# Optimization experiments

Measured on AMD Instinct MI355X. Metric: run time of the kernel, lower is better.

## Reference

```python
import jax, jax.numpy as jnp
import numpy as np

EMBED_DIM = 768
NUM_HEADS = 12
DILATION_RATES = [1, 2, 4]
SEGMENT_LENGTHS = [2048, 4096, 8192]
LN_EPS = 1e-5
CAUSAL = False


def _dilated_attention(q, k, v, causal=False):
    # q, k, v: (b, N, h, d)
    b, N, h, d = q.shape
    g = len(DILATION_RATES)
    gs = h // g
    scale = 1.0 / jnp.sqrt(jnp.asarray(d, q.dtype))
    out = jnp.zeros_like(q)
    for i, (r, s) in enumerate(zip(DILATION_RATES, SEGMENT_LENGTHS)):
        n = N // s
        offset = i % r
        hmin, hmax = i * gs, (i + 1) * gs
        # strided gather: (b, n, s_eff, gs, d)
        qi = q.reshape(b, n, s, h, d)[:, :, offset::r, hmin:hmax, :]
        ki = k.reshape(b, n, s, h, d)[:, :, offset::r, hmin:hmax, :]
        vi = v.reshape(b, n, s, h, d)[:, :, offset::r, hmin:hmax, :]
        scores = jnp.einsum('bnqhd,bnkhd->bnhqk', qi, ki) * scale
        if causal:
            s_eff = qi.shape[2]
            mask = jnp.tril(jnp.ones((s_eff, s_eff), dtype=bool))
            scores = jnp.where(mask, scores, jnp.asarray(-jnp.inf, scores.dtype))
        p = jax.nn.softmax(scores, axis=-1)
        x = jnp.einsum('bnhqk,bnkhd->bnqhd', p, vi)
        # original normalization: divide by sum over (segment, position) dims
        x = x / x.sum(axis=(1, 2), keepdims=True)
        out = (out.reshape(b, n, s, h, d)
                  .at[:, :, offset::r, hmin:hmax, :].add(x)
                  .reshape(b, N, h, d))
    return out / g


def setup_inputs() -> dict:
    key = jax.random.key(0)
    ks = jax.random.split(key, 13)
    b, N, E = 2, 8192, EMBED_DIM
    sd = 1.0 / np.sqrt(E)
    return {
        'query': jax.random.normal(ks[0], (b, N, E), jnp.float32),
        'key': jax.random.normal(ks[1], (b, N, E), jnp.float32),
        'value': jax.random.normal(ks[2], (b, N, E), jnp.float32),
        'Wq': jax.random.normal(ks[3], (E, E), jnp.float32) * sd,
        'bq': jnp.zeros((E,), jnp.float32),
        'Wk': jax.random.normal(ks[4], (E, E), jnp.float32) * sd,
        'bk': jnp.zeros((E,), jnp.float32),
        'Wv': jax.random.normal(ks[5], (E, E), jnp.float32) * sd,
        'bv': jnp.zeros((E,), jnp.float32),
        'Wo': jax.random.normal(ks[6], (E, E), jnp.float32) * sd,
        'bo': jnp.zeros((E,), jnp.float32),
        'ln_w': jnp.ones((E,), jnp.float32),
        'ln_b': jnp.zeros((E,), jnp.float32),
    }


def reference(query, key, value, Wq, bq, Wk, bk, Wv, bv, Wo, bo, ln_w, ln_b):
    b, N, E = query.shape
    h = NUM_HEADS
    d = E // h
    q = (query @ Wq + bq).reshape(b, N, h, d)
    k = (key @ Wk + bk).reshape(b, N, h, d)
    v = (value @ Wv + bv).reshape(b, N, h, d)
    x = _dilated_attention(q, k, v, causal=CAUSAL).reshape(b, N, E)
    mu = x.mean(axis=-1, keepdims=True)
    var = x.var(axis=-1, keepdims=True)
    x = (x - mu) / jnp.sqrt(var + LN_EPS) * ln_w + ln_b
    return x @ Wo + bo
```

## Files before the change

### kernel.cpp

```cpp
#include <hip/hip_runtime.h>

typedef __attribute__((ext_vector_type(4))) float f32x4;
typedef __attribute__((ext_vector_type(4))) unsigned int u32x4;
typedef __attribute__((ext_vector_type(8))) _Float16 half8;
typedef __attribute__((ext_vector_type(2))) _Float16 half2v;

__device__ inline f32x4 mfma_fp16(half8 a, half8 b, f32x4 c) {
  return __builtin_amdgcn_mfma_f32_16x16x32_f16(a, b, c, 0, 0, 0);
}

__device__ inline int kva(int row, int colbyte) {
  return ((row * 128 + colbyte) ^ ((row & 7) << 4)) >> 1;
}

__device__ inline void gload16(const _Float16* g, _Float16* l) {
  __builtin_amdgcn_global_load_lds(
      (const __attribute__((address_space(1))) void*)g,
      (__attribute__((address_space(3))) void*)l, 16, 0, 0);
}

__global__ __launch_bounds__(256) void wsplit4_kernel(
    const float* __restrict__ Wq, const float* __restrict__ Wk,
    const float* __restrict__ Wv, const float* __restrict__ Wo,
    _Float16* __restrict__ Whi, _Float16* __restrict__ Wlo) {
  int w = blockIdx.y;
  const float* W = (w == 0) ? Wq : (w == 1) ? Wk : (w == 2) ? Wv : Wo;
  int i = blockIdx.x * 256 + threadIdx.x;
  int k = i / 768, n = i % 768;
  float v = W[i];
  _Float16 h = (_Float16)v;
  Whi[w * 589824 + n * 768 + k] = h;
  Wlo[w * 589824 + n * 768 + k] = (_Float16)(v - (float)h);
}

__device__ inline void asplit_body(const float* __restrict__ A,
                                   _Float16* __restrict__ Ahi,
                                   _Float16* __restrict__ Alo, int i) {
  f32x4 x0 = *(const f32x4*)(A + i);
  f32x4 x1 = *(const f32x4*)(A + i + 4);
  half8 vh, vl;
#pragma unroll
  for (int j = 0; j < 4; ++j) {
    _Float16 h0 = (_Float16)x0[j];
    vh[j] = h0; vl[j] = (_Float16)(x0[j] - (float)h0);
    _Float16 h1 = (_Float16)x1[j];
    vh[4 + j] = h1; vl[4 + j] = (_Float16)(x1[j] - (float)h1);
  }
  *(half8*)(Ahi + i) = vh;
  *(half8*)(Alo + i) = vl;
}

__global__ __launch_bounds__(256) void asplit_kernel(const float* __restrict__ A,
                                                     _Float16* __restrict__ Ahi,
                                                     _Float16* __restrict__ Alo) {
  asplit_body(A, Ahi, Alo, (blockIdx.x * 256 + threadIdx.x) * 8);
}

__global__ __launch_bounds__(256) void asplit3_kernel(
    const float* __restrict__ Aq, const float* __restrict__ Ak,
    const float* __restrict__ Av,
    _Float16* __restrict__ Aqh, _Float16* __restrict__ Aql,
    _Float16* __restrict__ Akh, _Float16* __restrict__ Akl,
    _Float16* __restrict__ Avh, _Float16* __restrict__ Avl) {
  int w = blockIdx.y;
  const float* A = (w == 0) ? Aq : (w == 1) ? Ak : Av;
  _Float16* H = (w == 0) ? Aqh : (w == 1) ? Akh : Avh;
  _Float16* L = (w == 0) ? Aql : (w == 1) ? Akl : Avl;
  asplit_body(A, H, L, (blockIdx.x * 256 + threadIdx.x) * 8);
}

__device__ inline int vt_base(int b, int h) {
  int base = b * 3670016;
  if (h < 4)      base += h * 524288;
  else if (h < 8) base += 2097152 + (h - 4) * 262144;
  else            base += 3145728 + (h - 8) * 131072;
  return base;
}

__device__ __forceinline__ void gemm3_core(
    const _Float16* __restrict__ Ahi, const _Float16* __restrict__ Alo,
    const _Float16* __restrict__ Bhi, const _Float16* __restrict__ Blo,
    const float* __restrict__ bias, _Float16* __restrict__ Chi,
    _Float16* __restrict__ Clo, int mode, int m0, int n0,
    _Float16* Ah, _Float16* Al, _Float16* Bh, _Float16* Bl) {
  int tid = threadIdx.x;
  int lane = tid & 63, wid = tid >> 6;
  int wm = wid >> 1, wn = wid & 1;
  int lg = lane >> 4, lc = lane & 15;

  f32x4 acc[2][4] = {};

  size_t sA[2], sB[2];
  int ldst[2];
#pragma unroll
  for (int c = 0; c < 2; ++c) {
    int idxv = c * 512 + tid;
    int m = idxv >> 3;
    int ke = ((idxv & 7) << 3) ^ ((m & 7) << 3);
    sA[c] = (size_t)(m0 + m) * 768 + ke;
    sB[c] = (size_t)(n0 + m) * 768 + ke;
    ldst[c] = (c * 512 + wid * 64) * 8;
  }

  for (int k0 = 0; k0 < 768; k0 += 64) {
    __syncthreads();
#pragma unroll
    for (int c = 0; c < 2; ++c) {
      gload16(Ahi + sA[c] + k0, Ah + ldst[c]);
      gload16(Alo + sA[c] + k0, Al + ldst[c]);
      gload16(Bhi + sB[c] + k0, Bh + ldst[c]);
      gload16(Blo + sB[c] + k0, Bl + ldst[c]);
    }
    __syncthreads();

#pragma unroll
    for (int ks = 0; ks < 2; ++ks) {
      half8 ah[2], al[2], bh[4], bl[4];
#pragma unroll
      for (int mt = 0; mt < 2; ++mt) {
        int ro = kva(wm * 32 + mt * 16 + lc, ks * 64 + (lg << 4));
        ah[mt] = *(half8*)(&Ah[ro]);
        al[mt] = *(half8*)(&Al[ro]);
      }
#pragma unroll
      for (int nf = 0; nf < 4; ++nf) {
        int ro = kva(wn * 64 + nf * 16 + lc, ks * 64 + (lg << 4));
        bh[nf] = *(half8*)(&Bh[ro]);
        bl[nf] = *(half8*)(&Bl[ro]);
      }
#pragma unroll
      for (int mt = 0; mt < 2; ++mt)
#pragma unroll
        for (int nf = 0; nf < 4; ++nf) {
          acc[mt][nf] = mfma_fp16(al[mt], bh[nf], acc[mt][nf]);
          acc[mt][nf] = mfma_fp16(ah[mt], bl[nf], acc[mt][nf]);
          acc[mt][nf] = mfma_fp16(ah[mt], bh[nf], acc[mt][nf]);
        }
    }
  }

#pragma unroll
  for (int mt = 0; mt < 2; ++mt)
#pragma unroll
    for (int nf = 0; nf < 4; ++nf) {
      int col = n0 + wn * 64 + nf * 16 + lc;
      int row0 = m0 + wm * 32 + mt * 16 + (lg << 2);
      float bv = bias[col];
#pragma unroll
      for (int rr = 0; rr < 4; ++rr) {
        int row = row0 + rr;
        float v = acc[mt][nf][rr] + bv;
        _Float16 h = (_Float16)v;
        _Float16 l = (_Float16)(v - (float)h);
        if (mode == 0) {
          Chi[(size_t)row * 768 + col] = h;
          Clo[(size_t)row * 768 + col] = l;
        } else {
          int b = row >> 13, pos = row & 8191;
          int hh = col >> 6, d = col & 63;
          int g = hh >> 2;
          int rdil = 1 << g;
          if ((pos & (rdil - 1)) == g) {
            int t = (pos - g) >> g;
            int Ng = 8192 >> g;
            Chi[vt_base(b, hh) + d * Ng + t] = h;
            Clo[vt_base(b, hh) + d * Ng + t] = l;
          }
        }
      }
    }
}

__global__ __launch_bounds__(512, 2) void gemm3_kernel(
    const _Float16* __restrict__ Ahi, const _Float16* __restrict__ Alo,
    const _Float16* __restrict__ Bhi, const _Float16* __restrict__ Blo,
    const float* __restrict__ bias,
    _Float16* __restrict__ Chi, _Float16* __restrict__ Clo, int mode) {
  __shared__ _Float16 Ah[128 * 64], Al[128 * 64], Bh[128 * 64], Bl[128 * 64];
  gemm3_core(Ahi, Alo, Bhi, Blo, bias, Chi, Clo, mode,
             blockIdx.y * 128, blockIdx.x * 128, Ah, Al, Bh, Bl);
}

__global__ __launch_bounds__(512, 2) void gemm3b_kernel(
    const _Float16* __restrict__ Aqh, const _Float16* __restrict__ Aql,
    const _Float16* __restrict__ Akh, const _Float16* __restrict__ Akl,
    const _Float16* __restrict__ Avh, const _Float16* __restrict__ Avl,
    const _Float16* __restrict__ Wsh, const _Float16* __restrict__ Wsl,
    const float* __restrict__ bq, const float* __restrict__ bk,
    const float* __restrict__ bv,
    _Float16* __restrict__ Qhb, _Float16* __restrict__ Qlb,
    _Float16* __restrict__ Khb, _Float16* __restrict__ Klb,
    _Float16* __restrict__ Vth, _Float16* __restrict__ Vtl) {
  __shared__ _Float16 Ah[128 * 64], Al[128 * 64], Bh[128 * 64], Bl[128 * 64];
  int orig = blockIdx.x;
  int wg = (orig & 7) * 288 + (orig >> 3);
  int sec = wg / 768, rem = wg % 768;
  int m0 = (rem / 6) * 128, n0 = (rem % 6) * 128;
  const _Float16* Ahi = (sec == 0) ? Aqh : (sec == 1) ? Akh : Avh;
  const _Float16* Alo = (sec == 0) ? Aql : (sec == 1) ? Akl : Avl;
  const float* bias = (sec == 0) ? bq : (sec == 1) ? bk : bv;
  _Float16* Chi = (sec == 0) ? Qhb : (sec == 1) ? Khb : Vth;
  _Float16* Clo = (sec == 0) ? Qlb : (sec == 1) ? Klb : Vtl;
  gemm3_core(Ahi, Alo, Wsh + sec * 589824, Wsl + sec * 589824, bias,
             Chi, Clo, (sec == 2) ? 1 : 0, m0, n0, Ah, Al, Bh, Bl);
}

__global__ __launch_bounds__(256, 4) void gemm1_kernel(
    const _Float16* __restrict__ A, const _Float16* __restrict__ Bt,
    const float* __restrict__ bias, float* __restrict__ C) {
  __shared__ _Float16 As[128 * 64];
  __shared__ _Float16 Bs[128 * 64];
  int orig = blockIdx.x;
  int wg = (orig & 7) * 96 + (orig >> 3);
  int m0 = (wg / 6) * 128, n0 = (wg % 6) * 128;
  int tid = threadIdx.x;
  int lane = tid & 63, wid = tid >> 6;
  int wm = wid >> 1, wn = wid & 1;
  int lg = lane >> 4, lc = lane & 15;

  f32x4 acc[4][4] = {};

  size_t sA[4], sB[4];
  int ldst[4];
#pragma unroll
  for (int c = 0; c < 4; ++c) {
    int idxv = c * 256 + tid;
    int m = idxv >> 3;
    int ke = ((idxv & 7) << 3) ^ ((m & 7) << 3);
    sA[c] = (size_t)(m0 + m) * 768 + ke;
    sB[c] = (size_t)(n0 + m) * 768 + ke;
    ldst[c] = (c * 256 + wid * 64) * 8;
  }

  for (int k0 = 0; k0 < 768; k0 += 64) {
    __syncthreads();
#pragma unroll
    for (int c = 0; c < 4; ++c) {
      gload16(A + sA[c] + k0, As + ldst[c]);
      gload16(Bt + sB[c] + k0, Bs + ldst[c]);
    }
    __syncthreads();
#pragma unroll
    for (int ks = 0; ks < 2; ++ks) {
      half8 af[4], bf[4];
#pragma unroll
      for (int mt = 0; mt < 4; ++mt)
        af[mt] = *(half8*)(&As[kva(wm * 64 + mt * 16 + lc, ks * 64 + (lg << 4))]);
#pragma unroll
      for (int nf = 0; nf < 4; ++nf)
        bf[nf] = *(half8*)(&Bs[kva(wn * 64 + nf * 16 + lc, ks * 64 + (lg << 4))]);
#pragma unroll
      for (int mt = 0; mt < 4; ++mt)
#pragma unroll
        for (int nf = 0; nf < 4; ++nf)
          acc[mt][nf] = mfma_fp16(af[mt], bf[nf], acc[mt][nf]);
    }
  }

#pragma unroll
  for (int mt = 0; mt < 4; ++mt)
#pragma unroll
    for (int nf = 0; nf < 4; ++nf) {
      int col = n0 + wn * 64 + nf * 16 + lc;
      int row0 = m0 + wm * 64 + mt * 16 + (lg << 2);
      float bv = bias[col];
#pragma unroll
      for (int rr = 0; rr < 4; ++rr)
        C[(size_t)(row0 + rr) * 768 + col] = acc[mt][nf][rr] + bv;
    }
}

__global__ __launch_bounds__(512, 4) void attn_kernel(
    const _Float16* __restrict__ Qh, const _Float16* __restrict__ Ql,
    const _Float16* __restrict__ Kh, const _Float16* __restrict__ Kl,
    const _Float16* __restrict__ Vth, const _Float16* __restrict__ Vtl,
    _Float16* __restrict__ Xh, float* __restrict__ partial) {
  __shared__ _Float16 Ksh[64 * 64], Ksl[64 * 64];
  __shared__ _Float16 Vsh[64 * 64], Vsl[64 * 64];
  __shared__ float wred[8][64];

  int bid = blockIdx.x;
  int xcd = bid & 7, idx = bid >> 3;
  int u_glob = xcd * 7 + (idx >> 4);
  int qblk = idx & 15;
  int g = (u_glob < 32) ? 0 : (u_glob < 48) ? 1 : 2;
  int u = (g == 0) ? u_glob : (g == 1) ? u_glob - 32 : u_glob - 48;
  int nsegs = 4 >> g;
  int b = u / (nsegs * 4), rem = u % (nsegs * 4);
  int nseg = rem >> 2, hg = rem & 3;
  int head = g * 4 + hg;
  int s = 2048 << g, r = 1 << g, off = g;
  int Ng = 8192 >> g;
  int tbase = nseg * 2048;
  int vbase = vt_base(b, head);

  int tid = threadIdx.x, lane = tid & 63, wid = tid >> 6;
  int lg = lane >> 4, lc = lane & 15;

  int q0 = qblk * 128 + wid * 16;
  half8 qfh[2], qfl[2];
  {
    int q = q0 + lc;
    int pos = nseg * s + off + q * r;
    size_t ro = (size_t)(b * 8192 + pos) * 768 + head * 64;
#pragma unroll
    for (int ks = 0; ks < 2; ++ks) {
      qfh[ks] = *(const half8*)(Qh + ro + ks * 32 + (lg << 3));
      qfl[ks] = *(const half8*)(Ql + ro + ks * 32 + (lg << 3));
    }
  }

  int kr = tid >> 3, kcb = (tid & 7) << 4;
  const int kc = (tid & 7) << 3;
  size_t kro = (size_t)(b * 8192 + nseg * s + off + kr * r) * 768 + head * 64 + kc;
  size_t vro = (size_t)vbase + (size_t)kr * Ng + tbase + kc;
  const size_t kstep = (size_t)64 * r * 768;
  _Float16* KshW = &Ksh[kva(kr, kcb)];
  _Float16* KslW = &Ksl[kva(kr, kcb)];
  _Float16* VshW = &Vsh[kva(kr, kcb)];
  _Float16* VslW = &Vsl[kva(kr, kcb)];

  f32x4 acch[4] = {};
  float lsum = 0.f;

  const int sl0 = ((lane & 16) << 1) + lc;
  const int sl1 = sl0 + 16;
  const bool hiSel = (lane & 32) != 0;

  half8 rKh = *(const half8*)(Kh + kro);
  half8 rKl = *(const half8*)(Kl + kro);
  half8 rVh = *(const half8*)(Vth + vro);
  half8 rVl = *(const half8*)(Vtl + vro);
  kro += kstep;
  vro += 64;

  for (int kt = 0; kt < 32; ++kt) {
    __syncthreads();
    *(half8*)KshW = rKh;
    *(half8*)KslW = rKl;
    *(half8*)VshW = rVh;
    *(half8*)VslW = rVl;
    if (kt < 31) {
      rKh = *(const half8*)(Kh + kro);
      rKl = *(const half8*)(Kl + kro);
      rVh = *(const half8*)(Vth + vro);
      rVl = *(const half8*)(Vtl + vro);
      kro += kstep;
      vro += 64;
    }
    __syncthreads();

    f32x4 sc[4];
#pragma unroll
    for (int nf = 0; nf < 4; ++nf) {
      half8 kh[2], kl[2];
#pragma unroll
      for (int ks = 0; ks < 2; ++ks) {
        int ro = kva(nf * 16 + lc, ks * 64 + (lg << 4));
        kh[ks] = *(half8*)(&Ksh[ro]);
        kl[ks] = *(half8*)(&Ksl[ro]);
      }
      f32x4 t = {};
#pragma unroll
      for (int ks = 0; ks < 2; ++ks) {
        t = mfma_fp16(kl[ks], qfh[ks], t);
        t = mfma_fp16(kh[ks], qfl[ks], t);
      }
#pragma unroll
      for (int ks = 0; ks < 2; ++ks)
        t = mfma_fp16(kh[ks], qfh[ks], t);
      sc[nf] = t;
    }

    unsigned int pk[4][2];
#pragma unroll
    for (int nf = 0; nf < 4; ++nf) {
      _Float16 hh[4];
#pragma unroll
      for (int rr = 0; rr < 4; ++rr) {
        float p = __expf(sc[nf][rr] * 0.125f);
        hh[rr] = (_Float16)p;
        lsum += (float)hh[rr];
      }
      half2v p01 = {hh[0], hh[1]};
      half2v p23 = {hh[2], hh[3]};
      pk[nf][0] = __builtin_bit_cast(unsigned int, p01);
      pk[nf][1] = __builtin_bit_cast(unsigned int, p23);
    }

#pragma unroll
    for (int ks2 = 0; ks2 < 2; ++ks2) {
      int nfA = 2 * ks2, nfB = 2 * ks2 + 1;
      unsigned int a0 = __shfl(pk[nfA][0], sl0, 64);
      unsigned int b0 = __shfl(pk[nfB][0], sl0, 64);
      unsigned int a1 = __shfl(pk[nfA][1], sl0, 64);
      unsigned int b1 = __shfl(pk[nfB][1], sl0, 64);
      unsigned int a2 = __shfl(pk[nfA][0], sl1, 64);
      unsigned int b2 = __shfl(pk[nfB][0], sl1, 64);
      unsigned int a3 = __shfl(pk[nfA][1], sl1, 64);
      unsigned int b3 = __shfl(pk[nfB][1], sl1, 64);
      u32x4 pw;
      pw[0] = hiSel ? b0 : a0;
      pw[1] = hiSel ? b1 : a1;
      pw[2] = hiSel ? b2 : a2;
      pw[3] = hiSel ? b3 : a3;
      half8 pa = __builtin_bit_cast(half8, pw);
#pragma unroll
      for (int nf = 0; nf < 4; ++nf) {
        int ro = kva(nf * 16 + lc, ks2 * 64 + (lg << 4));
        half8 vh = *(half8*)(&Vsh[ro]);
        half8 vl = *(half8*)(&Vsl[ro]);
        acch[nf] = mfma_fp16(pa, vl, acch[nf]);
        acch[nf] = mfma_fp16(pa, vh, acch[nf]);
      }
    }
  }

  lsum += __shfl_xor(lsum, 16, 64);
  lsum += __shfl_xor(lsum, 32, 64);
  float inv_l = 1.0f / lsum;

  float cs[4] = {};
#pragma unroll
  for (int rr = 0; rr < 4; ++rr) {
    int qi = ((lane >> 4) & 3) * 4 + rr;
    float invq = __shfl(inv_l, (lane & 48) + qi, 64);
    int q = q0 + qi;
    int pos = nseg * s + off + q * r;
    _Float16* xr = Xh + (size_t)(b * 8192 + pos) * 768 + head * 64;
#pragma unroll
    for (int nf = 0; nf < 4; ++nf) {
      _Float16 hx = (_Float16)(acch[nf][rr] * invq);
      xr[nf * 16 + lc] = hx;
      cs[nf] += (float)hx;
    }
  }
#pragma unroll
  for (int nf = 0; nf < 4; ++nf) {
    cs[nf] += __shfl_xor(cs[nf], 16, 64);
    cs[nf] += __shfl_xor(cs[nf], 32, 64);
    if (lane < 16) wred[wid][nf * 16 + lc] = cs[nf];
  }
  __syncthreads();
  if (tid < 64) {
    float w4 = 0.f;
#pragma unroll
    for (int w = 0; w < 8; ++w) w4 += wred[w][tid];
    int slot = ((b * 12 + head) * 64 + nseg * 16 + qblk);
    partial[slot * 64 + tid] = w4;
  }
}

__global__ __launch_bounds__(256) void colsum2_kernel(const float* __restrict__ partial,
                                                      float* __restrict__ divbuf) {
  int i = blockIdx.x * 256 + threadIdx.x;
  int b = i / 768, e = i % 768;
  int h = e >> 6, d = e & 63;
  int g = h >> 2;
  int nslots = 64 >> g;
  const float* src = partial + (size_t)((b * 12 + h) * 64) * 64 + d;
  float sacc = 0.f;
  for (int c = 0; c < nslots; ++c) sacc += src[c * 64];
  divbuf[i] = sacc;
}

__global__ __launch_bounds__(256) void ln_kernel(const _Float16* __restrict__ Xh,
                                                 _Float16* __restrict__ Xln,
                                                 const float* __restrict__ divbuf,
                                                 const float* __restrict__ ln_w,
                                                 const float* __restrict__ ln_b) {
  int wid = threadIdx.x >> 6, lane = threadIdx.x & 63;
  int row = blockIdx.x * 4 + wid;
  int b = row >> 13, pos = row & 8191;
  float x[12];
  float s1 = 0.f, s2 = 0.f;
#pragma unroll
  for (int j = 0; j < 12; ++j) {
    int e = lane + 64 * j;
    int g = j >> 2;
    bool wr = (g == 0) || (g == 1 && (pos & 1) == 1) || (g == 2 && (pos & 3) == 2);
    float v = 0.f;
    if (wr) v = (float)Xh[(size_t)row * 768 + e] / (divbuf[b * 768 + e] * 3.0f);
    x[j] = v;
    s1 += v;
    s2 += v * v;
  }
#pragma unroll
  for (int msk = 1; msk < 64; msk <<= 1) {
    s1 += __shfl_xor(s1, msk, 64);
    s2 += __shfl_xor(s2, msk, 64);
  }
  float mean = s1 * (1.0f / 768.0f);
  float var = s2 * (1.0f / 768.0f) - mean * mean;
  float inv = rsqrtf(var + 1e-5f);
#pragma unroll
  for (int j = 0; j < 12; ++j) {
    int e = lane + 64 * j;
    Xln[(size_t)row * 768 + e] = (_Float16)((x[j] - mean) * inv * ln_w[e] + ln_b[e]);
  }
}

extern "C" void kernel_launch(void* const* d_in, const int* in_sizes, int n_in,
                              void* d_out, int out_size, void* d_ws, size_t ws_size,
                              hipStream_t stream) {
  const float* query = (const float*)d_in[0];
  const float* key   = (const float*)d_in[1];
  const float* value = (const float*)d_in[2];
  const float* Wq = (const float*)d_in[3];
  const float* bq = (const float*)d_in[4];
  const float* Wk = (const float*)d_in[5];
  const float* bk = (const float*)d_in[6];
  const float* Wv = (const float*)d_in[7];
  const float* bv = (const float*)d_in[8];
  const float* Wo = (const float*)d_in[9];
  const float* bo = (const float*)d_in[10];
  const float* ln_w = (const float*)d_in[11];
  const float* ln_b = (const float*)d_in[12];

  char* ws = (char*)d_ws;
  _Float16* Wsh = (_Float16*)ws; ws += (size_t)4 * 589824 * 2;
  _Float16* Wsl = (_Float16*)ws; ws += (size_t)4 * 589824 * 2;
  _Float16* Qhb = (_Float16*)ws; ws += (size_t)16384 * 768 * 2;
  _Float16* Qlb = (_Float16*)ws; ws += (size_t)16384 * 768 * 2;
  _Float16* Khb = (_Float16*)ws; ws += (size_t)16384 * 768 * 2;
  _Float16* Klb = (_Float16*)ws; ws += (size_t)16384 * 768 * 2;
  _Float16* Vth = (_Float16*)ws; ws += (size_t)7340032 * 2;
  _Float16* Vtl = (_Float16*)ws; ws += (size_t)7340032 * 2;
  char* Xregion = ws; ws += (size_t)16384 * 768 * 4;
  float* partial = (float*)ws; ws += (size_t)24 * 64 * 64 * 4;
  float* divbuf = (float*)ws; ws += 2 * 768 * 4;

  _Float16* Xh  = (_Float16*)Xregion;
  _Float16* Xln = Xh + (size_t)16384 * 768;
  _Float16* Aqh = (_Float16*)Xregion;
  _Float16* Aql = Aqh + (size_t)16384 * 768;

  size_t base_bytes = (size_t)(ws - (char*)d_ws);
  size_t extra = (size_t)4 * 16384 * 768 * 2;
  bool batched = ws_size >= base_bytes + extra;

  wsplit4_kernel<<<dim3(2304, 4), 256, 0, stream>>>(Wq, Wk, Wv, Wo, Wsh, Wsl);

  dim3 ggrid(6, 128);
  if (batched) {
    _Float16* Akh = (_Float16*)ws; ws += (size_t)16384 * 768 * 2;
    _Float16* Akl = (_Float16*)ws; ws += (size_t)16384 * 768 * 2;
    _Float16* Avh = (_Float16*)ws; ws += (size_t)16384 * 768 * 2;
    _Float16* Avl = (_Float16*)ws; ws += (size_t)16384 * 768 * 2;
    asplit3_kernel<<<dim3(6144, 3), 256, 0, stream>>>(query, key, value,
        Aqh, Aql, Akh, Akl, Avh, Avl);
    gemm3b_kernel<<<2304, 512, 0, stream>>>(
        Aqh, Aql, Akh, Akl, Avh, Avl, Wsh, Wsl, bq, bk, bv,
        Qhb, Qlb, Khb, Klb, Vth, Vtl);
  } else {
    asplit_kernel<<<6144, 256, 0, stream>>>(query, Aqh, Aql);
    gemm3_kernel<<<ggrid, 512, 0, stream>>>(Aqh, Aql, Wsh, Wsl, bq, Qhb, Qlb, 0);
    asplit_kernel<<<6144, 256, 0, stream>>>(key, Aqh, Aql);
    gemm3_kernel<<<ggrid, 512, 0, stream>>>(Aqh, Aql, Wsh + 589824, Wsl + 589824, bk, Khb, Klb, 0);
    asplit_kernel<<<6144, 256, 0, stream>>>(value, Aqh, Aql);
    gemm3_kernel<<<ggrid, 512, 0, stream>>>(Aqh, Aql, Wsh + 2 * 589824, Wsl + 2 * 589824, bv, Vth, Vtl, 1);
  }

  attn_kernel<<<896, 512, 0, stream>>>(Qhb, Qlb, Khb, Klb, Vth, Vtl, Xh, partial);

  colsum2_kernel<<<6, 256, 0, stream>>>(partial, divbuf);
  ln_kernel<<<4096, 256, 0, stream>>>(Xh, Xln, divbuf, ln_w, ln_b);

  gemm1_kernel<<<768, 256, 0, stream>>>(Xln, Wsh + 3 * 589824, bo, (float*)d_out);
}
```

Baseline: 617.1 us.

## Give each attention wave two query tiles and load K/V directly into LDS

```diff
diff --git a/kernel.cpp b/kernel.cpp
--- a/kernel.cpp
+++ b/kernel.cpp
@@ -270,14 +270,14 @@
     }
 }
 
-__global__ __launch_bounds__(512, 4) void attn_kernel(
+__global__ __launch_bounds__(256, 3) void attn_kernel(
     const _Float16* __restrict__ Qh, const _Float16* __restrict__ Ql,
     const _Float16* __restrict__ Kh, const _Float16* __restrict__ Kl,
     const _Float16* __restrict__ Vth, const _Float16* __restrict__ Vtl,
     _Float16* __restrict__ Xh, float* __restrict__ partial) {
   __shared__ _Float16 Ksh[64 * 64], Ksl[64 * 64];
   __shared__ _Float16 Vsh[64 * 64], Vsl[64 * 64];
-  __shared__ float wred[8][64];
+  __shared__ float wred[4][64];
 
   int bid = blockIdx.x;
   int xcd = bid & 7, idx = bid >> 3;
@@ -297,60 +297,57 @@
   int tid = threadIdx.x, lane = tid & 63, wid = tid >> 6;
   int lg = lane >> 4, lc = lane & 15;
 
-  int q0 = qblk * 128 + wid * 16;
-  half8 qfh[2], qfl[2];
+  int q0 = qblk * 128 + wid * 32;
+  half8 qAh[2], qAl[2], qBh[2], qBl[2];
   {
-    int q = q0 + lc;
-    int pos = nseg * s + off + q * r;
-    size_t ro = (size_t)(b * 8192 + pos) * 768 + head * 64;
+    int posA = nseg * s + off + (q0 + lc) * r;
+    int posB = nseg * s + off + (q0 + 16 + lc) * r;
+    size_t roA = (size_t)(b * 8192 + posA) * 768 + head * 64;
+    size_t roB = (size_t)(b * 8192 + posB) * 768 + head * 64;
 #pragma unroll
     for (int ks = 0; ks < 2; ++ks) {
-      qfh[ks] = *(const half8*)(Qh + ro + ks * 32 + (lg << 3));
-      qfl[ks] = *(const half8*)(Ql + ro + ks * 32 + (lg << 3));
-    }
-  }
-
-  int kr = tid >> 3, kcb = (tid & 7) << 4;
-  const int kc = (tid & 7) << 3;
-  size_t kro = (size_t)(b * 8192 + nseg * s + off + kr * r) * 768 + head * 64 + kc;
-  size_t vro = (size_t)vbase + (size_t)kr * Ng + tbase + kc;
+      qAh[ks] = *(const half8*)(Qh + roA + ks * 32 + (lg << 3));
+      qAl[ks] = *(const half8*)(Ql + roA + ks * 32 + (lg << 3));
+      qBh[ks] = *(const half8*)(Qh + roB + ks * 32 + (lg << 3));
+      qBl[ks] = *(const half8*)(Ql + roB + ks * 32 + (lg << 3));
+    }
+  }
+
+  int krl = (lane >> 3);
+  int ke = (((lane & 7) ^ krl) << 3);
+  size_t kro[2], vro[2];
+  int ldk[2];
+#pragma unroll
+  for (int c = 0; c < 2; ++c) {
+    int kr = c * 32 + wid * 8 + krl;
+    kro[c] = (size_t)(b * 8192 + nseg * s + off + kr * r) * 768 + head * 64 + ke;
+    vro[c] = (size_t)vbase + (size_t)kr * Ng + tbase + ke;
+    ldk[c] = c * 2048 + wid * 512;
+  }
   const size_t kstep = (size_t)64 * r * 768;
-  _Float16* KshW = &Ksh[kva(kr, kcb)];
-  _Float16* KslW = &Ksl[kva(kr, kcb)];
-  _Float16* VshW = &Vsh[kva(kr, kcb)];
-  _Float16* VslW = &Vsl[kva(kr, kcb)];
-
-  f32x4 acch[4] = {};
-  float lsum = 0.f;
+
+  f32x4 accA[4] = {};
+  f32x4 accB[4] = {};
+  float lsumA = 0.f, lsumB = 0.f;
 
   const int sl0 = ((lane & 16) << 1) + lc;
   const int sl1 = sl0 + 16;
   const bool hiSel = (lane & 32) != 0;
 
-  half8 rKh = *(const half8*)(Kh + kro);
-  half8 rKl = *(const half8*)(Kl + kro);
-  half8 rVh = *(const half8*)(Vth + vro);
-  half8 rVl = *(const half8*)(Vtl + vro);
-  kro += kstep;
-  vro += 64;
-
   for (int kt = 0; kt < 32; ++kt) {
     __syncthreads();
-    *(half8*)KshW = rKh;
-    *(half8*)KslW = rKl;
-    *(half8*)VshW = rVh;
-    *(half8*)VslW = rVl;
-    if (kt < 31) {
-      rKh = *(const half8*)(Kh + kro);
-      rKl = *(const half8*)(Kl + kro);
-      rVh = *(const half8*)(Vth + vro);
-      rVl = *(const half8*)(Vtl + vro);
-      kro += kstep;
-      vro += 64;
+#pragma unroll
+    for (int c = 0; c < 2; ++c) {
+      gload16(Kh + kro[c], Ksh + ldk[c]);
+      gload16(Kl + kro[c], Ksl + ldk[c]);
+      gload16(Vth + vro[c], Vsh + ldk[c]);
+      gload16(Vtl + vro[c], Vsl + ldk[c]);
+      kro[c] += kstep;
+      vro[c] += 64;
     }
     __syncthreads();
 
-    f32x4 sc[4];
+    unsigned int pkA[4][2], pkB[4][2];
 #pragma unroll
     for (int nf = 0; nf < 4; ++nf) {
       half8 kh[2], kl[2];
@@ -360,79 +357,105 @@
         kh[ks] = *(half8*)(&Ksh[ro]);
         kl[ks] = *(half8*)(&Ksl[ro]);
       }
-      f32x4 t = {};
+      f32x4 tA = {}, tB = {};
 #pragma unroll
       for (int ks = 0; ks < 2; ++ks) {
-        t = mfma_fp16(kl[ks], qfh[ks], t);
-        t = mfma_fp16(kh[ks], qfl[ks], t);
-      }
-#pragma unroll
-      for (int ks = 0; ks < 2; ++ks)
-        t = mfma_fp16(kh[ks], qfh[ks], t);
-      sc[nf] = t;
-    }
-
-    unsigned int pk[4][2];
-#pragma unroll
-    for (int nf = 0; nf < 4; ++nf) {
-      _Float16 hh[4];
+        tA = mfma_fp16(kl[ks], qAh[ks], tA);
+        tA = mfma_fp16(kh[ks], qAl[ks], tA);
+        tB = mfma_fp16(kl[ks], qBh[ks], tB);
+        tB = mfma_fp16(kh[ks], qBl[ks], tB);
+      }
+#pragma unroll
+      for (int ks = 0; ks < 2; ++ks) {
+        tA = mfma_fp16(kh[ks], qAh[ks], tA);
+        tB = mfma_fp16(kh[ks], qBh[ks], tB);
+      }
+      _Float16 hA[4], hB[4];
 #pragma unroll
       for (int rr = 0; rr < 4; ++rr) {
-        float p = __expf(sc[nf][rr] * 0.125f);
-        hh[rr] = (_Float16)p;
-        lsum += (float)hh[rr];
-      }
-      half2v p01 = {hh[0], hh[1]};
-      half2v p23 = {hh[2], hh[3]};
-      pk[nf][0] = __builtin_bit_cast(unsigned int, p01);
-      pk[nf][1] = __builtin_bit_cast(unsigned int, p23);
+        float pA = __expf(tA[rr] * 0.125f);
+        float pB = __expf(tB[rr] * 0.125f);
+        hA[rr] = (_Float16)pA; lsumA += (float)hA[rr];
+        hB[rr] = (_Float16)pB; lsumB += (float)hB[rr];
+      }
+      half2v a01 = {hA[0], hA[1]}, a23 = {hA[2], hA[3]};
+      half2v b01 = {hB[0], hB[1]}, b23 = {hB[2], hB[3]};
+      pkA[nf][0] = __builtin_bit_cast(unsigned int, a01);
+      pkA[nf][1] = __builtin_bit_cast(unsigned int, a23);
+      pkB[nf][0] = __builtin_bit_cast(unsigned int, b01);
+      pkB[nf][1] = __builtin_bit_cast(unsigned int, b23);
     }
 
 #pragma unroll
     for (int ks2 = 0; ks2 < 2; ++ks2) {
       int nfA = 2 * ks2, nfB = 2 * ks2 + 1;
-      unsigned int a0 = __shfl(pk[nfA][0], sl0, 64);
-      unsigned int b0 = __shfl(pk[nfB][0], sl0, 64);
-      unsigned int a1 = __shfl(pk[nfA][1], sl0, 64);
-      unsigned int b1 = __shfl(pk[nfB][1], sl0, 64);
-      unsigned int a2 = __shfl(pk[nfA][0], sl1, 64);
-      unsigned int b2 = __shfl(pk[nfB][0], sl1, 64);
-      unsigned int a3 = __shfl(pk[nfA][1], sl1, 64);
-      unsigned int b3 = __shfl(pk[nfB][1], sl1, 64);
-      u32x4 pw;
-      pw[0] = hiSel ? b0 : a0;
-      pw[1] = hiSel ? b1 : a1;
-      pw[2] = hiSel ? b2 : a2;
-      pw[3] = hiSel ? b3 : a3;
-      half8 pa = __builtin_bit_cast(half8, pw);
+      unsigned int aA0 = __shfl(pkA[nfA][0], sl0, 64);
+      unsigned int aB0 = __shfl(pkA[nfB][0], sl0, 64);
+      unsigned int aA1 = __shfl(pkA[nfA][1], sl0, 64);
+      unsigned int aB1 = __shfl(pkA[nfB][1], sl0, 64);
+      unsigned int aA2 = __shfl(pkA[nfA][0], sl1, 64);
+      unsigned int aB2 = __shfl(pkA[nfB][0], sl1, 64);
+      unsigned int aA3 = __shfl(pkA[nfA][1], sl1, 64);
+      unsigned int aB3 = __shfl(pkA[nfB][1], sl1, 64);
+      u32x4 pwA;
+      pwA[0] = hiSel ? aB0 : aA0;
+      pwA[1] = hiSel ? aB1 : aA1;
+      pwA[2] = hiSel ? aB2 : aA2;
+      pwA[3] = hiSel ? aB3 : aA3;
+      half8 paA = __builtin_bit_cast(half8, pwA);
+
+      unsigned int bA0 = __shfl(pkB[nfA][0], sl0, 64);
+      unsigned int bB0 = __shfl(pkB[nfB][0], sl0, 64);
+      unsigned int bA1 = __shfl(pkB[nfA][1], sl0, 64);
+      unsigned int bB1 = __shfl(pkB[nfB][1], sl0, 64);
+      unsigned int bA2 = __shfl(pkB[nfA][0], sl1, 64);
+      unsigned int bB2 = __shfl(pkB[nfB][0], sl1, 64);
+      unsigned int bA3 = __shfl(pkB[nfA][1], sl1, 64);
+      unsigned int bB3 = __shfl(pkB[nfB][1], sl1, 64);
+      u32x4 pwB;
+      pwB[0] = hiSel ? bB0 : bA0;
+      pwB[1] = hiSel ? bB1 : bA1;
+      pwB[2] = hiSel ? bB2 : bA2;
+      pwB[3] = hiSel ? bB3 : bA3;
+      half8 paB = __builtin_bit_cast(half8, pwB);
+
 #pragma unroll
       for (int nf = 0; nf < 4; ++nf) {
         int ro = kva(nf * 16 + lc, ks2 * 64 + (lg << 4));
         half8 vh = *(half8*)(&Vsh[ro]);
         half8 vl = *(half8*)(&Vsl[ro]);
-        acch[nf] = mfma_fp16(pa, vl, acch[nf]);
-        acch[nf] = mfma_fp16(pa, vh, acch[nf]);
-      }
-    }
-  }
-
-  lsum += __shfl_xor(lsum, 16, 64);
-  lsum += __shfl_xor(lsum, 32, 64);
-  float inv_l = 1.0f / lsum;
+        accA[nf] = mfma_fp16(paA, vl, accA[nf]);
+        accA[nf] = mfma_fp16(paA, vh, accA[nf]);
+        accB[nf] = mfma_fp16(paB, vl, accB[nf]);
+        accB[nf] = mfma_fp16(paB, vh, accB[nf]);
+      }
+    }
+  }
+
+  lsumA += __shfl_xor(lsumA, 16, 64);
+  lsumA += __shfl_xor(lsumA, 32, 64);
+  lsumB += __shfl_xor(lsumB, 16, 64);
+  lsumB += __shfl_xor(lsumB, 32, 64);
+  float invA = 1.0f / lsumA;
+  float invB = 1.0f / lsumB;
 
   float cs[4] = {};
 #pragma unroll
   for (int rr = 0; rr < 4; ++rr) {
     int qi = ((lane >> 4) & 3) * 4 + rr;
-    float invq = __shfl(inv_l, (lane & 48) + qi, 64);
-    int q = q0 + qi;
-    int pos = nseg * s + off + q * r;
-    _Float16* xr = Xh + (size_t)(b * 8192 + pos) * 768 + head * 64;
+    float invqA = __shfl(invA, (lane & 48) + qi, 64);
+    float invqB = __shfl(invB, (lane & 48) + qi, 64);
+    int posA = nseg * s + off + (q0 + qi) * r;
+    int posB = nseg * s + off + (q0 + 16 + qi) * r;
+    _Float16* xrA = Xh + (size_t)(b * 8192 + posA) * 768 + head * 64;
+    _Float16* xrB = Xh + (size_t)(b * 8192 + posB) * 768 + head * 64;
 #pragma unroll
     for (int nf = 0; nf < 4; ++nf) {
-      _Float16 hx = (_Float16)(acch[nf][rr] * invq);
-      xr[nf * 16 + lc] = hx;
-      cs[nf] += (float)hx;
+      _Float16 hxA = (_Float16)(accA[nf][rr] * invqA);
+      _Float16 hxB = (_Float16)(accB[nf][rr] * invqB);
+      xrA[nf * 16 + lc] = hxA;
+      xrB[nf * 16 + lc] = hxB;
+      cs[nf] += (float)hxA + (float)hxB;
     }
   }
 #pragma unroll
@@ -443,9 +466,7 @@
   }
   __syncthreads();
   if (tid < 64) {
-    float w4 = 0.f;
-#pragma unroll
-    for (int w = 0; w < 8; ++w) w4 += wred[w][tid];
+    float w4 = wred[0][tid] + wred[1][tid] + wred[2][tid] + wred[3][tid];
     int slot = ((b * 12 + head) * 64 + nseg * 16 + qblk);
     partial[slot * 64 + tid] = w4;
   }
@@ -561,7 +582,7 @@
     gemm3_kernel<<<ggrid, 512, 0, stream>>>(Aqh, Aql, Wsh + 2 * 589824, Wsl + 2 * 589824, bv, Vth, Vtl, 1);
   }
 
-  attn_kernel<<<896, 512, 0, stream>>>(Qhb, Qlb, Khb, Klb, Vth, Vtl, Xh, partial);
+  attn_kernel<<<896, 256, 0, stream>>>(Qhb, Qlb, Khb, Klb, Vth, Vtl, Xh, partial);
 
   colsum2_kernel<<<6, 256, 0, stream>>>(partial, divbuf);
   ln_kernel<<<4096, 256, 0, stream>>>(Xh, Xln, divbuf, ln_w, ln_b);
```

New measurement: 629.2 us. No clear change (+2.0%).
